# Kernel tuning notes

Measured on AMD Instinct MI355X. Metric: run time of the kernel, lower is better.

Reference implementation:

```python
import jax, jax.numpy as jnp
import numpy as np

C = 256
CR = 32  # C // nc_reduce

def setup_inputs() -> dict:
    key = jax.random.key(0)
    ks = jax.random.split(key, 8)
    B, H, W = 4, 64, 64
    x = jax.random.normal(ks[0], (B, C, H, W), dtype=jnp.float32)
    s_in = 1.0 / np.sqrt(C)
    Wq = jax.random.uniform(ks[1], (CR, C), jnp.float32, -s_in, s_in)
    bq = jax.random.uniform(ks[2], (CR,), jnp.float32, -s_in, s_in)
    Wk = jax.random.uniform(ks[3], (CR, C), jnp.float32, -s_in, s_in)
    bk = jax.random.uniform(ks[4], (CR,), jnp.float32, -s_in, s_in)
    Wv = jax.random.uniform(ks[5], (C, C), jnp.float32, -s_in, s_in)
    bv = jax.random.uniform(ks[6], (C,), jnp.float32, -s_in, s_in)
    gamma = jnp.zeros((1,), dtype=jnp.float32)
    return {"x": x, "Wq": Wq, "bq": bq, "Wk": Wk, "bk": bk,
            "Wv": Wv, "bv": bv, "gamma": gamma}

def reference(x, Wq, bq, Wk, bk, Wv, bv, gamma):
    B, Cc, H, W = x.shape
    N = H * W
    xf = x.reshape(B, Cc, N)                       # [B, C, N]
    # 1x1 convs == per-position channel projections
    q = jnp.einsum('dc,bcn->bdn', Wq, xf) + bq[None, :, None]  # [B, CR, N]
    k = jnp.einsum('dc,bcn->bdn', Wk, xf) + bk[None, :, None]  # [B, CR, N]
    v = jnp.einsum('dc,bcn->bdn', Wv, xf) + bv[None, :, None]  # [B, C, N]
    # energy[b,i,j] = q[:, :, i] . k[:, :, j]  (no scaling, as in source)
    energy = jnp.einsum('bdi,bdj->bij', q, k)      # [B, N, N]
    attn = jax.nn.softmax(energy, axis=-1)
    # out[b,c,i] = sum_j v[b,c,j] * attn[b,i,j]
    outv = jnp.einsum('bcj,bij->bci', v, attn)     # [B, C, N]
    out = gamma[0] * outv.reshape(B, Cc, H, W) + x
    return out
```

## Files before the change

kernel.cpp:

```cpp
#include <hip/hip_runtime.h>
#include <hip/hip_bf16.h>

#define NB 4
#define CCH 256
#define CRD 32
#define NN 4096

typedef __attribute__((ext_vector_type(8))) short short8;
typedef __attribute__((ext_vector_type(4))) float floatx4;
typedef __attribute__((ext_vector_type(4))) int intx4;
typedef __attribute__((ext_vector_type(2))) unsigned int uintx2;

__device__ __forceinline__ unsigned short f2bf(float f) {
  unsigned u = __builtin_bit_cast(unsigned, f);
  u += 0x7FFFu + ((u >> 16) & 1u);
  return (unsigned short)(u >> 16);
}

__device__ __forceinline__ unsigned short f2bf_c(float f) {
  f = fminf(fmaxf(f, -1.0e4f), 1.0e4f);
  unsigned u = __builtin_bit_cast(unsigned, f);
  u += 0x7FFFu + ((u >> 16) & 1u);
  return (unsigned short)(u >> 16);
}

__device__ __forceinline__ unsigned pack2c(float a, float b) {
  return (unsigned)f2bf_c(a) | ((unsigned)f2bf_c(b) << 16);
}

__device__ __forceinline__ float sat(float v) {
  return fminf(fmaxf(v, -1.0e30f), 1.0e30f);
}

__device__ __forceinline__ short8 ld_frag_g(const unsigned short* p) {
  return __builtin_bit_cast(short8, *(const intx4*)p);
}

__global__ __launch_bounds__(256) void gemm_qkv_fused(
    const float* __restrict__ x,
    const float* __restrict__ Wq, const float* __restrict__ bq,
    const float* __restrict__ Wk, const float* __restrict__ bk,
    const float* __restrict__ Wv, const float* __restrict__ bv,
    unsigned short* __restrict__ qT, unsigned short* __restrict__ kT,
    unsigned short* __restrict__ vv)
{
  __shared__ __align__(16) unsigned short xs[64 * 264];
  __shared__ __align__(16) unsigned short ws[64 * 264];

  const int tid  = threadIdx.x;
  const int wave = tid >> 6;
  const int lane = tid & 63;
  const int lq   = lane >> 4;
  const int lm   = lane & 15;
  const int n0   = blockIdx.x << 6;
  const int mg   = blockIdx.y;
  const int b    = blockIdx.z;

  {
    const int nn = lane;
    const int cg = wave;
    const float* xb = x + ((size_t)b << 20) + n0 + nn;
#pragma unroll
    for (int it = 0; it < 16; ++it) {
      const int c0 = it * 16 + cg * 4;
      const float v0 = xb[(size_t)(c0 + 0) << 12];
      const float v1 = xb[(size_t)(c0 + 1) << 12];
      const float v2 = xb[(size_t)(c0 + 2) << 12];
      const float v3 = xb[(size_t)(c0 + 3) << 12];
      uintx2 u;
      u[0] = pack2c(v0, v1);
      u[1] = pack2c(v2, v3);
      *(uintx2*)(xs + nn * 264 + c0) = u;
    }
  }

  const int mt_lo = mg ? 3 : 0;
  const int mt_hi = mg ? 5 : 3;

  for (int mt = mt_lo; mt < mt_hi; ++mt) {
#pragma unroll
    for (int i = 0; i < 16; ++i) {
      const int u  = i * 256 + tid;
      const int m  = u >> 6;
      const int o4 = (u & 63) * 4;
      const float* src = (mt == 0)
          ? (m < 32 ? Wq + (size_t)m * CCH : Wk + (size_t)(m - 32) * CCH)
          : Wv + (size_t)((mt - 1) * 64 + m) * CCH;
      const floatx4 f = *(const floatx4*)(src + o4);
      uintx2 uu;
      uu[0] = pack2c(f[0], f[1]);
      uu[1] = pack2c(f[2], f[3]);
      *(uintx2*)(ws + m * 264 + o4) = uu;
    }
    __syncthreads();

    floatx4 acc[4];
#pragma unroll
    for (int t = 0; t < 4; ++t) acc[t] = (floatx4){0.f, 0.f, 0.f, 0.f};

#pragma unroll
    for (int k0 = 0; k0 < 8; ++k0) {
      short8 af[4];
#pragma unroll
      for (int ms = 0; ms < 4; ++ms)
        af[ms] = __builtin_bit_cast(short8,
            *(const intx4*)(ws + (ms * 16 + lm) * 264 + k0 * 32 + lq * 8));
      const short8 bf = __builtin_bit_cast(short8,
          *(const intx4*)(xs + (wave * 16 + lm) * 264 + k0 * 32 + lq * 8));
#pragma unroll
      for (int ms = 0; ms < 4; ++ms)
        acc[ms] = __builtin_amdgcn_mfma_f32_16x16x32_bf16(af[ms], bf,
                                                          acc[ms], 0, 0, 0);
    }
    __syncthreads();

    if (mt == 0) {
      const int n = n0 + wave * 16 + lm;
#pragma unroll
      for (int ms = 0; ms < 4; ++ms) {
        const int d0 = (ms & 1) * 16 + lq * 4;
        const float* bias = (ms < 2) ? bq : bk;
        unsigned short* dst = (ms < 2) ? qT : kT;
        uintx2 u;
        u[0] = pack2c(acc[ms][0] + bias[d0],     acc[ms][1] + bias[d0 + 1]);
        u[1] = pack2c(acc[ms][2] + bias[d0 + 2], acc[ms][3] + bias[d0 + 3]);
        *(uintx2*)(dst + (size_t)(b * NN + n) * CRD + d0) = u;
      }
    } else {
      const int cb = (mt - 1) * 64;
      unsigned short* vb2 = ws;
#pragma unroll
      for (int ms = 0; ms < 4; ++ms)
#pragma unroll
        for (int r = 0; r < 4; ++r) {
          const int c = ms * 16 + lq * 4 + r;
          vb2[c * 64 + wave * 16 + lm] = f2bf_c(acc[ms][r] + bv[cb + c]);
        }
      __syncthreads();
#pragma unroll
      for (int it = 0; it < 2; ++it) {
        const int u = it * 256 + tid;
        const int m = u >> 3;
        const int o = (u & 7) * 8;
        *(intx4*)(vv + (size_t)(b * CCH + cb + m) * NN + n0 + o) =
            *(const intx4*)(vb2 + m * 64 + o);
      }
      __syncthreads();
    }
  }
}

__global__ __launch_bounds__(1024) void attn_kernel(
    const float* __restrict__ x, const float* __restrict__ gamma_p,
    const unsigned short* __restrict__ qT, const unsigned short* __restrict__ kT,
    const unsigned short* __restrict__ vv, float* __restrict__ out)
{
  __shared__ __align__(16) unsigned char smem[65536 + 2 * 4 * 2176];

  const int tid  = threadIdx.x;
  const int wave = tid >> 6;
  const int wg   = wave >> 2;
  const int cs   = wave & 3;
  const int lane = tid & 63;
  const int lq   = lane >> 4;
  const int lm   = lane & 15;
  const int xcd = blockIdx.x & 7;
  const int pos = blockIdx.x >> 3;
  const int b   = xcd >> 1;
  const int i0  = (((xcd & 1) << 5) | pos) << 6;

  const unsigned short* kTb = kT + (size_t)b * NN * CRD;
  const unsigned short* vb  = vv + (size_t)b * CCH * NN;

  const short8 qf =
      ld_frag_g(qT + (size_t)(b * NN + i0 + wg * 16 + lm) * CRD + lq * 8);

  int vs_g[2];
  int vs_off[2];
#pragma unroll
  for (int m = 0; m < 2; ++m) {
    const int u  = m * 1024 + tid;
    const int c  = u >> 3;
    const int jb = u & 7;
    vs_g[m]   = c * NN + jb * 8;
    vs_off[m] = c * 128 + ((jb ^ (c & 7)) * 16);
  }

  floatx4 acc[4];
#pragma unroll
  for (int t = 0; t < 4; ++t) acc[t] = (floatx4){0.f, 0.f, 0.f, 0.f};
  float lsum[4] = {0.f, 0.f, 0.f, 0.f};

  const floatx4 zf = {0.f, 0.f, 0.f, 0.f};

  intx4 vreg[2];
#pragma unroll
  for (int m = 0; m < 2; ++m)
    vreg[m] = *(const intx4*)(vb + vs_g[m]);
  short8 kf = ld_frag_g(kTb + (size_t)(cs * 16 + lm) * CRD + lq * 8);

#pragma unroll
  for (int m = 0; m < 2; ++m)
    *(intx4*)(smem + vs_off[m]) = vreg[m];
  {
    unsigned char* pb0 = smem + 65536 + wg * 2176;
    const floatx4 S = __builtin_amdgcn_mfma_f32_16x16x32_bf16(
        qf, kf, zf, 0, 0, 0);
#pragma unroll
    for (int r = 0; r < 4; ++r) {
      const float p = __expf(fminf(fmaxf(S[r], -40.f), 40.f));
      lsum[r] += p;
      *(unsigned short*)(pb0 + (lq * 4 + r) * 136 +
                         ((cs * 16 + lm) << 1)) = f2bf(p);
    }
  }
#pragma unroll
  for (int m = 0; m < 2; ++m)
    vreg[m] = *(const intx4*)(vb + vs_g[m] + 64);
  kf = ld_frag_g(kTb + (size_t)(64 + cs * 16 + lm) * CRD + lq * 8);

#pragma unroll 1
  for (int k = 0; k < 63; ++k) {
    asm volatile("s_waitcnt lgkmcnt(0)" ::: "memory");
    __builtin_amdgcn_s_barrier();

    unsigned char* vbp = smem + ((k & 1) << 15);
    unsigned char* pbp = smem + 65536 + (k & 1) * 8704 + wg * 2176;
    unsigned char* vbn = smem + (((k + 1) & 1) << 15);
    unsigned char* pbn = smem + 65536 + ((k + 1) & 1) * 8704 + wg * 2176;

#pragma unroll
    for (int m = 0; m < 2; ++m)
      *(intx4*)(vbn + vs_off[m]) = vreg[m];

    {
      const floatx4 S = __builtin_amdgcn_mfma_f32_16x16x32_bf16(
          qf, kf, zf, 0, 0, 0);
#pragma unroll
      for (int r = 0; r < 4; ++r) {
        const float p = __expf(fminf(fmaxf(S[r], -40.f), 40.f));
        lsum[r] += p;
        *(unsigned short*)(pbn + (lq * 4 + r) * 136 +
                           ((cs * 16 + lm) << 1)) = f2bf(p);
      }
    }

    {
      const int j2 = ((k + 2 < 64) ? (k + 2) : 63) << 6;
#pragma unroll
      for (int m = 0; m < 2; ++m)
        vreg[m] = *(const intx4*)(vb + vs_g[m] + j2);
      kf = ld_frag_g(kTb + (size_t)(j2 + cs * 16 + lm) * CRD + lq * 8);
    }

#pragma unroll
    for (int ks = 0; ks < 2; ++ks) {
      const unsigned char* pa = pbp + lm * 136 + ks * 64 + lq * 16;
      struct U128 { unsigned long long a, b; } pp;
      pp.a = *(const unsigned long long*)pa;
      pp.b = *(const unsigned long long*)(pa + 8);
      const short8 pf = __builtin_bit_cast(short8, pp);
#pragma unroll
      for (int nt = 0; nt < 4; ++nt) {
        const int c = cs * 64 + nt * 16 + lm;
        const short8 vf = __builtin_bit_cast(
            short8,
            *(const intx4*)(vbp + c * 128 + (((ks * 4 + lq) ^ (lm & 7)) * 16)));
        acc[nt] = __builtin_amdgcn_mfma_f32_16x16x32_bf16(pf, vf, acc[nt],
                                                          0, 0, 0);
      }
    }
  }

  asm volatile("s_waitcnt lgkmcnt(0)" ::: "memory");
  __builtin_amdgcn_s_barrier();
  {
    const unsigned char* vbp = smem + (1 << 15);
    const unsigned char* pbp = smem + 65536 + 8704 + wg * 2176;
#pragma unroll
    for (int ks = 0; ks < 2; ++ks) {
      const unsigned char* pa = pbp + lm * 136 + ks * 64 + lq * 16;
      struct U128 { unsigned long long a, b; } pp;
      pp.a = *(const unsigned long long*)pa;
      pp.b = *(const unsigned long long*)(pa + 8);
      const short8 pf = __builtin_bit_cast(short8, pp);
#pragma unroll
      for (int nt = 0; nt < 4; ++nt) {
        const int c = cs * 64 + nt * 16 + lm;
        const short8 vf = __builtin_bit_cast(
            short8,
            *(const intx4*)(vbp + c * 128 + (((ks * 4 + lq) ^ (lm & 7)) * 16)));
        acc[nt] = __builtin_amdgcn_mfma_f32_16x16x32_bf16(pf, vf, acc[nt],
                                                          0, 0, 0);
      }
    }
  }

#pragma unroll
  for (int r = 0; r < 4; ++r) {
    float v = lsum[r];
    v += __shfl_xor(v, 1);
    v += __shfl_xor(v, 2);
    v += __shfl_xor(v, 4);
    v += __shfl_xor(v, 8);
    lsum[r] = v;
  }
  __syncthreads();
  {
    floatx4 lv;
#pragma unroll
    for (int r = 0; r < 4; ++r) lv[r] = lsum[r];
    *(floatx4*)(smem + ((wave * 64 + lane) << 4)) = lv;
  }
  __syncthreads();
  float inv[4];
  {
    floatx4 s = {0.f, 0.f, 0.f, 0.f};
#pragma unroll
    for (int q = 0; q < 4; ++q) {
      const floatx4 lp =
          *(const floatx4*)(smem + (((wg * 4 + q) * 64 + lane) << 4));
      s = s + lp;
    }
#pragma unroll
    for (int r = 0; r < 4; ++r) inv[r] = 1.0f / s[r];
  }

  __syncthreads();
  float* olds = (float*)smem;
  {
    const int ib = wg * 16 + lq * 4;
#pragma unroll
    for (int nt = 0; nt < 4; ++nt) {
      const int c = cs * 64 + nt * 16 + lm;
      floatx4 o;
#pragma unroll
      for (int r = 0; r < 4; ++r) o[r] = sat(acc[nt][r] * inv[r]);
      *(floatx4*)(olds + c * 68 + ib) = o;
    }
  }
  __syncthreads();

  const float gm = gamma_p[0];
#pragma unroll
  for (int pass = 0; pass < 4; ++pass) {
    const int c  = pass * 64 + (tid >> 4);
    const int i4 = (tid & 15) * 4;
    const floatx4 ov = *(const floatx4*)(olds + c * 68 + i4);
    const size_t idx = (size_t)(b * CCH + c) * NN + i0 + i4;
    const floatx4 xv = *(const floatx4*)(x + idx);
    floatx4 o;
#pragma unroll
    for (int e = 0; e < 4; ++e)
      o[e] = gm * ov[e] + xv[e];
    *(floatx4*)(out + idx) = o;
  }
}

extern "C" void kernel_launch(void* const* d_in, const int* in_sizes, int n_in,
                              void* d_out, int out_size, void* d_ws, size_t ws_size,
                              hipStream_t stream) {
  (void)in_sizes; (void)n_in; (void)out_size; (void)ws_size;
  const float* x     = (const float*)d_in[0];
  const float* Wq    = (const float*)d_in[1];
  const float* bq    = (const float*)d_in[2];
  const float* Wk    = (const float*)d_in[3];
  const float* bk    = (const float*)d_in[4];
  const float* Wv    = (const float*)d_in[5];
  const float* bv    = (const float*)d_in[6];
  const float* gamma = (const float*)d_in[7];

  unsigned short* qT = (unsigned short*)d_ws;
  unsigned short* kT = qT + (size_t)NB * NN * CRD;
  unsigned short* vv = kT + (size_t)NB * NN * CRD;

  gemm_qkv_fused<<<dim3(64, 2, 4), 256, 0, stream>>>(x, Wq, bq, Wk, bk, Wv, bv,
                                                     qT, kT, vv);
  attn_kernel<<<dim3(256, 1, 1), 1024, 0, stream>>>(x, gamma, qT, kT, vv,
                                                    (float*)d_out);
}
```

Baseline: 156.7 us.

## Split PV reduction across wave pairs so each V fragment feeds two row tiles

Waves are regrouped so each one handles two 16-row query tiles and one half of the 64-key block, instead of one row tile and the full key block. Each V fragment read from LDS now feeds two MFMAs, halving V LDS reads per MFMA. The cost is doubled accumulator registers and an extra combine step, where the two key halves are added through shared memory with an additional barrier. Because the result is split across two partial sums, it also adds a little floating-point reordering.

```diff
diff --git a/kernel.cpp b/kernel.cpp
--- a/kernel.cpp
+++ b/kernel.cpp
@@ -159,8 +159,10 @@
 
   const int tid  = threadIdx.x;
   const int wave = tid >> 6;
-  const int wg   = wave >> 2;
-  const int cs   = wave & 3;
+  const int ig   = wave >> 3;
+  const int cs   = (wave >> 1) & 3;
+  const int js   = wave & 1;
+  const int it   = ig * 2 + js;
   const int lane = tid & 63;
   const int lq   = lane >> 4;
   const int lm   = lane & 15;
@@ -173,7 +175,7 @@
   const unsigned short* vb  = vv + (size_t)b * CCH * NN;
 
   const short8 qf =
-      ld_frag_g(qT + (size_t)(b * NN + i0 + wg * 16 + lm) * CRD + lq * 8);
+      ld_frag_g(qT + (size_t)(b * NN + i0 + it * 16 + lm) * CRD + lq * 8);
 
   int vs_g[2];
   int vs_off[2];
@@ -186,9 +188,9 @@
     vs_off[m] = c * 128 + ((jb ^ (c & 7)) * 16);
   }
 
-  floatx4 acc[4];
-#pragma unroll
-  for (int t = 0; t < 4; ++t) acc[t] = (floatx4){0.f, 0.f, 0.f, 0.f};
+  floatx4 acc[8];
+#pragma unroll
+  for (int t = 0; t < 8; ++t) acc[t] = (floatx4){0.f, 0.f, 0.f, 0.f};
   float lsum[4] = {0.f, 0.f, 0.f, 0.f};
 
   const floatx4 zf = {0.f, 0.f, 0.f, 0.f};
@@ -203,7 +205,7 @@
   for (int m = 0; m < 2; ++m)
     *(intx4*)(smem + vs_off[m]) = vreg[m];
   {
-    unsigned char* pb0 = smem + 65536 + wg * 2176;
+    unsigned char* pb0 = smem + 65536 + it * 2176;
     const floatx4 S = __builtin_amdgcn_mfma_f32_16x16x32_bf16(
         qf, kf, zf, 0, 0, 0);
 #pragma unroll
@@ -225,9 +227,9 @@
     __builtin_amdgcn_s_barrier();
 
     unsigned char* vbp = smem + ((k & 1) << 15);
-    unsigned char* pbp = smem + 65536 + (k & 1) * 8704 + wg * 2176;
+    unsigned char* ppar = smem + 65536 + (k & 1) * 8704;
     unsigned char* vbn = smem + (((k + 1) & 1) << 15);
-    unsigned char* pbn = smem + 65536 + ((k + 1) & 1) * 8704 + wg * 2176;
+    unsigned char* pnxt = smem + 65536 + ((k + 1) & 1) * 8704;
 
 #pragma unroll
     for (int m = 0; m < 2; ++m)
@@ -236,6 +238,7 @@
     {
       const floatx4 S = __builtin_amdgcn_mfma_f32_16x16x32_bf16(
           qf, kf, zf, 0, 0, 0);
+      unsigned char* pbn = pnxt + it * 2176;
 #pragma unroll
       for (int r = 0; r < 4; ++r) {
         const float p = __expf(fminf(fmaxf(S[r], -40.f), 40.f));
@@ -253,21 +256,27 @@
       kf = ld_frag_g(kTb + (size_t)(j2 + cs * 16 + lm) * CRD + lq * 8);
     }
 
-#pragma unroll
-    for (int ks = 0; ks < 2; ++ks) {
-      const unsigned char* pa = pbp + lm * 136 + ks * 64 + lq * 16;
-      struct U128 { unsigned long long a, b; } pp;
-      pp.a = *(const unsigned long long*)pa;
-      pp.b = *(const unsigned long long*)(pa + 8);
-      const short8 pf = __builtin_bit_cast(short8, pp);
+    {
+      short8 pf[2];
+#pragma unroll
+      for (int f = 0; f < 2; ++f) {
+        const unsigned char* pa =
+            ppar + (ig * 2 + f) * 2176 + lm * 136 + js * 64 + lq * 16;
+        struct U128 { unsigned long long a, b; } pp;
+        pp.a = *(const unsigned long long*)pa;
+        pp.b = *(const unsigned long long*)(pa + 8);
+        pf[f] = __builtin_bit_cast(short8, pp);
+      }
 #pragma unroll
       for (int nt = 0; nt < 4; ++nt) {
         const int c = cs * 64 + nt * 16 + lm;
         const short8 vf = __builtin_bit_cast(
             short8,
-            *(const intx4*)(vbp + c * 128 + (((ks * 4 + lq) ^ (lm & 7)) * 16)));
-        acc[nt] = __builtin_amdgcn_mfma_f32_16x16x32_bf16(pf, vf, acc[nt],
-                                                          0, 0, 0);
+            *(const intx4*)(vbp + c * 128 + (((js * 4 + lq) ^ (lm & 7)) * 16)));
+#pragma unroll
+        for (int f = 0; f < 2; ++f)
+          acc[f * 4 + nt] = __builtin_amdgcn_mfma_f32_16x16x32_bf16(
+              pf[f], vf, acc[f * 4 + nt], 0, 0, 0);
       }
     }
   }
@@ -276,23 +285,27 @@
   __builtin_amdgcn_s_barrier();
   {
     const unsigned char* vbp = smem + (1 << 15);
-    const unsigned char* pbp = smem + 65536 + 8704 + wg * 2176;
-#pragma unroll
-    for (int ks = 0; ks < 2; ++ks) {
-      const unsigned char* pa = pbp + lm * 136 + ks * 64 + lq * 16;
+    const unsigned char* ppar = smem + 65536 + 8704;
+    short8 pf[2];
+#pragma unroll
+    for (int f = 0; f < 2; ++f) {
+      const unsigned char* pa =
+          ppar + (ig * 2 + f) * 2176 + lm * 136 + js * 64 + lq * 16;
       struct U128 { unsigned long long a, b; } pp;
       pp.a = *(const unsigned long long*)pa;
       pp.b = *(const unsigned long long*)(pa + 8);
-      const short8 pf = __builtin_bit_cast(short8, pp);
-#pragma unroll
-      for (int nt = 0; nt < 4; ++nt) {
-        const int c = cs * 64 + nt * 16 + lm;
-        const short8 vf = __builtin_bit_cast(
-            short8,
-            *(const intx4*)(vbp + c * 128 + (((ks * 4 + lq) ^ (lm & 7)) * 16)));
-        acc[nt] = __builtin_amdgcn_mfma_f32_16x16x32_bf16(pf, vf, acc[nt],
-                                                          0, 0, 0);
-      }
+      pf[f] = __builtin_bit_cast(short8, pp);
+    }
+#pragma unroll
+    for (int nt = 0; nt < 4; ++nt) {
+      const int c = cs * 64 + nt * 16 + lm;
+      const short8 vf = __builtin_bit_cast(
+          short8,
+          *(const intx4*)(vbp + c * 128 + (((js * 4 + lq) ^ (lm & 7)) * 16)));
+#pragma unroll
+      for (int f = 0; f < 2; ++f)
+        acc[f * 4 + nt] = __builtin_amdgcn_mfma_f32_16x16x32_bf16(
+            pf[f], vf, acc[f * 4 + nt], 0, 0, 0);
     }
   }
 
@@ -310,34 +323,53 @@
     floatx4 lv;
 #pragma unroll
     for (int r = 0; r < 4; ++r) lv[r] = lsum[r];
-    *(floatx4*)(smem + ((wave * 64 + lane) << 4)) = lv;
+    *(floatx4*)(smem + (((it * 4 + cs) * 64 + lane) << 4)) = lv;
   }
   __syncthreads();
-  float inv[4];
-  {
+  floatx4 invf[2];
+#pragma unroll
+  for (int f = 0; f < 2; ++f) {
     floatx4 s = {0.f, 0.f, 0.f, 0.f};
 #pragma unroll
     for (int q = 0; q < 4; ++q) {
-      const floatx4 lp =
-          *(const floatx4*)(smem + (((wg * 4 + q) * 64 + lane) << 4));
+      const floatx4 lp = *(const floatx4*)(
+          smem + ((((ig * 2 + f) * 4 + q) * 64 + lane) << 4));
       s = s + lp;
     }
 #pragma unroll
-    for (int r = 0; r < 4; ++r) inv[r] = 1.0f / s[r];
-  }
-
+    for (int r = 0; r < 4; ++r) invf[f][r] = 1.0f / s[r];
+  }
   __syncthreads();
+
   float* olds = (float*)smem;
-  {
-    const int ib = wg * 16 + lq * 4;
-#pragma unroll
-    for (int nt = 0; nt < 4; ++nt) {
-      const int c = cs * 64 + nt * 16 + lm;
-      floatx4 o;
-#pragma unroll
-      for (int r = 0; r < 4; ++r) o[r] = sat(acc[nt][r] * inv[r]);
-      *(floatx4*)(olds + c * 68 + ib) = o;
-    }
+  if (js == 0) {
+#pragma unroll
+    for (int f = 0; f < 2; ++f)
+#pragma unroll
+      for (int nt = 0; nt < 4; ++nt) {
+        const int c  = cs * 64 + nt * 16 + lm;
+        const int ib = (ig * 2 + f) * 16 + lq * 4;
+        floatx4 o;
+#pragma unroll
+        for (int r = 0; r < 4; ++r) o[r] = sat(acc[f * 4 + nt][r] * invf[f][r]);
+        *(floatx4*)(olds + c * 68 + ib) = o;
+      }
+  }
+  __syncthreads();
+  if (js == 1) {
+#pragma unroll
+    for (int f = 0; f < 2; ++f)
+#pragma unroll
+      for (int nt = 0; nt < 4; ++nt) {
+        const int c  = cs * 64 + nt * 16 + lm;
+        const int ib = (ig * 2 + f) * 16 + lq * 4;
+        float* dst = olds + c * 68 + ib;
+        floatx4 o = *(const floatx4*)dst;
+#pragma unroll
+        for (int r = 0; r < 4; ++r)
+          o[r] += sat(acc[f * 4 + nt][r] * invf[f][r]);
+        *(floatx4*)dst = o;
+      }
   }
   __syncthreads();
 
```

New measurement: 150.4 us. 1.04x faster.
